# Performance work log

Measured on AMD Instinct MI355X. Metric: run time of the kernel, lower is better.

## Reference

```python
import jax, jax.numpy as jnp
import numpy as np


def setup_inputs() -> dict:
    key = jax.random.key(0)
    k1, k2, k3, k4, k5 = jax.random.split(key, 5)
    N, M = 8192, 8192
    ref_kpts = jax.random.normal(k1, (N, 3), dtype=jnp.float32)
    src_kpts = jax.random.normal(k2, (M, 3), dtype=jnp.float32)
    gt_transform = jax.random.normal(k3, (4, 4), dtype=jnp.float32)
    ref_sigma = jax.random.uniform(k4, (N,), dtype=jnp.float32)
    src_sigma = jax.random.uniform(k5, (M,), dtype=jnp.float32)
    return {"ref_kpts": ref_kpts, "src_kpts": src_kpts, "gt_transform": gt_transform,
            "ref_sigma": ref_sigma, "src_sigma": src_sigma}


def reference(ref_kpts, src_kpts, gt_transform, ref_sigma, src_sigma):
    # apply_transform: rigid SE(3): p @ R^T + t
    R = gt_transform[:3, :3]
    t = gt_transform[:3, 3]
    kpts2 = src_kpts @ R.T + t  # [M, 3]
    # pairwise euclidean distances [N, M]
    diff = jnp.linalg.norm(ref_kpts[:, None, :] - kpts2[None, :, :], axis=-1)
    # forward direction: for each ref point, nearest transformed src point
    min_dist_fwd = jnp.min(diff, axis=-1)        # [N]
    idx_fwd = jnp.argmin(diff, axis=-1)          # [N]
    sigma_fwd = (ref_sigma + src_sigma[idx_fwd]) * 0.5
    forward_loss = jnp.mean(jnp.log(sigma_fwd) + min_dist_fwd / sigma_fwd)
    # backward direction: for each src point, nearest ref point
    min_dist_bwd = jnp.min(diff, axis=0)         # [M]
    idx_bwd = jnp.argmin(diff, axis=0)           # [M]
    sigma_bwd = (src_sigma + ref_sigma[idx_bwd]) * 0.5
    backward_loss = jnp.mean(jnp.log(sigma_bwd) + min_dist_bwd / sigma_bwd)
    return forward_loss + backward_loss
```

## Files before the change

### kernel.cpp

```cpp
#include <hip/hip_runtime.h>
#include <math.h>

typedef float v4f __attribute__((ext_vector_type(4)));

#define TPB 256
#define IPT 8
#define JS  128


__global__ __launch_bounds__(256) void setup_kernel(
    const float* __restrict__ ref, const float* __restrict__ src,
    const float* __restrict__ T,
    float* __restrict__ refI, float* __restrict__ srcI,
    unsigned long long* __restrict__ packF,
    unsigned long long* __restrict__ packB,
    float* __restrict__ out, int N, int M) {
  int i = blockIdx.x * blockDim.x + threadIdx.x;
  if (i < M) {
    float x = src[3 * i], y = src[3 * i + 1], z = src[3 * i + 2];
    float tx = T[0] * x + T[1] * y + T[2]  * z + T[3];
    float ty = T[4] * x + T[5] * y + T[6]  * z + T[7];
    float tz = T[8] * x + T[9] * y + T[10] * z + T[11];
    int base = 8 * (i >> 1) + (i & 1);
    srcI[base]     = tx;
    srcI[base + 2] = ty;
    srcI[base + 4] = tz;
    srcI[base + 6] = tx * tx + ty * ty + tz * tz;
    packB[i] = ~0ull;
  }
  if (i < N) {
    float x = ref[3 * i], y = ref[3 * i + 1], z = ref[3 * i + 2];
    int base = 8 * (i >> 1) + (i & 1);
    refI[base]     = x;
    refI[base + 2] = y;
    refI[base + 4] = z;
    refI[base + 6] = x * x + y * y + z * z;
    packF[i] = ~0ull;
  }
  if (i == 0) {
    out[0] = 0.0f;
#pragma unroll
    for (int e = 0; e < 2; e++) {
      int bn = 8 * ((N + e) >> 1) + ((N + e) & 1);
      refI[bn] = 0.f; refI[bn + 2] = 0.f; refI[bn + 4] = 0.f;
      refI[bn + 6] = 1e30f;
      int bm = 8 * ((M + e) >> 1) + ((M + e) & 1);
      srcI[bm] = 0.f; srcI[bm + 2] = 0.f; srcI[bm + 4] = 0.f;
      srcI[bm + 6] = 1e30f;
    }
  }
}

__device__ __forceinline__ unsigned int sortable(float f) {
  unsigned int u = __float_as_uint(f);
  return u ^ ((unsigned int)((int)u >> 31) | 0x80000000u);
}

__global__ __launch_bounds__(TPB, 4) void pairs_kernel(
    const float* __restrict__ refI, const float* __restrict__ srcI,
    unsigned long long* __restrict__ packF,
    unsigned long long* __restrict__ packB,
    int N, int M, int nbF) {
  int b = blockIdx.x;
  const float *selfI, *otherI;
  unsigned long long* pack;
  int selfN, otherN;
  if (b < nbF) {
    selfI = refI; otherI = srcI; pack = packF; selfN = N; otherN = M;
  } else {
    b -= nbF;
    selfI = srcI; otherI = refI; pack = packB; selfN = M; otherN = N;
  }
  const int ib = b / JS, jb = b % JS;
  const int i0 = ib * (TPB * IPT) + threadIdx.x;

  float ax[IPT], ay[IPT], az[IPT], m0[IPT], m1[IPT];
#pragma unroll
  for (int k = 0; k < IPT; k++) {
    int i = i0 + k * TPB;
    int ic = (i < selfN) ? i : (selfN - 1);
    int base = 8 * (ic >> 1) + (ic & 1);
    ax[k] = -2.0f * selfI[base];
    ay[k] = -2.0f * selfI[base + 2];
    az[k] = -2.0f * selfI[base + 4];
    m0[k] = 1e30f; m1[k] = 1e30f;
  }

  int chunk = (otherN + JS - 1) / JS;
  chunk = (chunk + 1) & ~1;
  const int j0 = jb * chunk;
  const int jcount = min(chunk, otherN - j0);

  const int lowbits = 32 - __clz((chunk > 2 ? chunk : 2) - 1);
  const unsigned keep = ~((1u << lowbits) - 1u);

  const v4f* og = (const v4f*)(otherI + 4 * j0);

#pragma unroll 2
  for (int jj = 0; jj < jcount; jj += 2) {
    v4f A = og[jj];
    v4f B = og[jj + 1];
#pragma unroll
    for (int k = 0; k < IPT; k++) {
      float u0 = __builtin_fmaf(ax[k], A.x, B.z);
      u0 = __builtin_fmaf(ay[k], A.z, u0);
      u0 = __builtin_fmaf(az[k], B.x, u0);
      float u1 = __builtin_fmaf(ax[k], A.y, B.w);
      u1 = __builtin_fmaf(ay[k], A.w, u1);
      u1 = __builtin_fmaf(az[k], B.y, u1);
      float e0 = __uint_as_float((__float_as_uint(u0) & keep) | (unsigned)jj);
      float e1 = __uint_as_float((__float_as_uint(u1) & keep) |
                                 (unsigned)(jj + 1));
      m0[k] = fminf(m0[k], e0);
      m1[k] = fminf(m1[k], e1);
    }
  }

#pragma unroll
  for (int k = 0; k < IPT; k++) {
    int i = i0 + k * TPB;
    if (i < selfN && jcount > 0) {
      float mf = fminf(m0[k], m1[k]);
      unsigned mb = __float_as_uint(mf);
      int jloc = (int)(mb & ~keep);
      unsigned long long p = ((unsigned long long)sortable(mf) << 32) |
                             (unsigned int)(j0 + jloc);
      atomicMin(&pack[i], p);
    }
  }
}

__global__ __launch_bounds__(256) void finalize_kernel(
    const unsigned long long* __restrict__ packF,
    const unsigned long long* __restrict__ packB,
    const float* __restrict__ refI, const float* __restrict__ srcI,
    const float* __restrict__ ref_sigma, const float* __restrict__ src_sigma,
    float* __restrict__ out, int N, int M) {
  int gid = blockIdx.x * blockDim.x + threadIdx.x;
  float term = 0.f;
  if (gid < N) {
    int idx = (int)(packF[gid] & 0xffffffffu);
    int sb = 8 * (gid >> 1) + (gid & 1);
    int ob = 8 * (idx >> 1) + (idx & 1);
    float dx = refI[sb]     - srcI[ob];
    float dy = refI[sb + 2] - srcI[ob + 2];
    float dz = refI[sb + 4] - srcI[ob + 4];
    float d = sqrtf(dx * dx + dy * dy + dz * dz);
    float sigma = 0.5f * (ref_sigma[gid] + src_sigma[idx]);
    term = (logf(sigma) + d / sigma) * (1.0f / (float)N);
  } else if (gid < N + M) {
    int j = gid - N;
    int idx = (int)(packB[j] & 0xffffffffu);
    int sb = 8 * (j >> 1) + (j & 1);
    int ob = 8 * (idx >> 1) + (idx & 1);
    float dx = srcI[sb]     - refI[ob];
    float dy = srcI[sb + 2] - refI[ob + 2];
    float dz = srcI[sb + 4] - refI[ob + 4];
    float d = sqrtf(dx * dx + dy * dy + dz * dz);
    float sigma = 0.5f * (src_sigma[j] + ref_sigma[idx]);
    term = (logf(sigma) + d / sigma) * (1.0f / (float)M);
  }
#pragma unroll
  for (int o = 32; o > 0; o >>= 1) term += __shfl_down(term, o, 64);
  __shared__ float wsum[4];
  const int lane = threadIdx.x & 63, wid = threadIdx.x >> 6;
  if (lane == 0) wsum[wid] = term;
  __syncthreads();
  if (threadIdx.x == 0)
    atomicAdd(out, wsum[0] + wsum[1] + wsum[2] + wsum[3]);
}

extern "C" void kernel_launch(void* const* d_in, const int* in_sizes, int n_in,
                              void* d_out, int out_size, void* d_ws,
                              size_t ws_size, hipStream_t stream) {
  const float* ref_kpts  = (const float*)d_in[0];
  const float* src_kpts  = (const float*)d_in[1];
  const float* gt        = (const float*)d_in[2];
  const float* ref_sigma = (const float*)d_in[3];
  const float* src_sigma = (const float*)d_in[4];
  float* out = (float*)d_out;

  const int N = in_sizes[0] / 3;
  const int M = in_sizes[1] / 3;

  const int NG8 = 8 * ((N + 3) / 2);
  const int MG8 = 8 * ((M + 3) / 2);
  float* f = (float*)d_ws;
  float* refI = f;
  float* srcI = f + NG8;
  unsigned long long* packF = (unsigned long long*)(f + NG8 + MG8);
  unsigned long long* packB = packF + N;

  int nPts = (N > M) ? N : M;
  setup_kernel<<<(nPts + 255) / 256, 256, 0, stream>>>(
      ref_kpts, src_kpts, gt, refI, srcI, packF, packB, out, N, M);

  const int ibF = (N + TPB * IPT - 1) / (TPB * IPT);
  const int ibB = (M + TPB * IPT - 1) / (TPB * IPT);
  const int nbF = ibF * JS;
  const int nbB = ibB * JS;
  pairs_kernel<<<nbF + nbB, TPB, 0, stream>>>(refI, srcI, packF, packB,
                                              N, M, nbF);

  finalize_kernel<<<(N + M + 255) / 256, 256, 0, stream>>>(
      packF, packB, refI, srcI, ref_sigma, src_sigma, out, N, M);
}
```

Baseline: 90.27 us.

## Fuse point transform into pairs kernel, stage tiles in LDS, replace atomics with partials

Drops the separate setup kernel. The pairs kernel now reads the raw ref/src points, applies the rigid transform on the fly, and stages each chunk of other-points with their squared norms into a shared-memory tile. Instead of 64-bit atomicMin into one packed array, each block writes its per-point min key to a partial buffer indexed by j-block. The finalize kernel reduces the 128 partials per point before computing the loss. This removes a launch and the atomic contention. In exchange it adds roughly 16 MB of partial-buffer traffic, redundant transform math in every block, and __syncthreads around the tile loads.

After: 92.66 us. 1.03x slower.

```diff
diff --git a/kernel.cpp b/kernel.cpp
--- a/kernel.cpp
+++ b/kernel.cpp
@@ -6,71 +6,52 @@
 #define TPB 256
 #define IPT 8
 #define JS  128
-
-
-__global__ __launch_bounds__(256) void setup_kernel(
-    const float* __restrict__ ref, const float* __restrict__ src,
-    const float* __restrict__ T,
-    float* __restrict__ refI, float* __restrict__ srcI,
-    unsigned long long* __restrict__ packF,
-    unsigned long long* __restrict__ packB,
-    float* __restrict__ out, int N, int M) {
-  int i = blockIdx.x * blockDim.x + threadIdx.x;
-  if (i < M) {
-    float x = src[3 * i], y = src[3 * i + 1], z = src[3 * i + 2];
-    float tx = T[0] * x + T[1] * y + T[2]  * z + T[3];
-    float ty = T[4] * x + T[5] * y + T[6]  * z + T[7];
-    float tz = T[8] * x + T[9] * y + T[10] * z + T[11];
-    int base = 8 * (i >> 1) + (i & 1);
-    srcI[base]     = tx;
-    srcI[base + 2] = ty;
-    srcI[base + 4] = tz;
-    srcI[base + 6] = tx * tx + ty * ty + tz * tz;
-    packB[i] = ~0ull;
-  }
-  if (i < N) {
-    float x = ref[3 * i], y = ref[3 * i + 1], z = ref[3 * i + 2];
-    int base = 8 * (i >> 1) + (i & 1);
-    refI[base]     = x;
-    refI[base + 2] = y;
-    refI[base + 4] = z;
-    refI[base + 6] = x * x + y * y + z * z;
-    packF[i] = ~0ull;
-  }
-  if (i == 0) {
-    out[0] = 0.0f;
-#pragma unroll
-    for (int e = 0; e < 2; e++) {
-      int bn = 8 * ((N + e) >> 1) + ((N + e) & 1);
-      refI[bn] = 0.f; refI[bn + 2] = 0.f; refI[bn + 4] = 0.f;
-      refI[bn + 6] = 1e30f;
-      int bm = 8 * ((M + e) >> 1) + ((M + e) & 1);
-      srcI[bm] = 0.f; srcI[bm + 2] = 0.f; srcI[bm + 4] = 0.f;
-      srcI[bm + 6] = 1e30f;
-    }
-  }
-}
+#define TS  512
+
 
 __device__ __forceinline__ unsigned int sortable(float f) {
   unsigned int u = __float_as_uint(f);
   return u ^ ((unsigned int)((int)u >> 31) | 0x80000000u);
 }
 
+struct Xform {
+  float t0, t1, t2, t3, t4, t5, t6, t7, t8, t9, t10, t11;
+};
+
+__device__ __forceinline__ Xform load_xform(const float* __restrict__ T) {
+  Xform X = {T[0], T[1], T[2], T[3], T[4],  T[5],
+             T[6], T[7], T[8], T[9], T[10], T[11]};
+  return X;
+}
+
+__device__ __forceinline__ void apply_xform(const Xform& X, float& x, float& y,
+                                            float& z) {
+  float tx = X.t0 * x + X.t1 * y + X.t2 * z + X.t3;
+  float ty = X.t4 * x + X.t5 * y + X.t6 * z + X.t7;
+  float tz = X.t8 * x + X.t9 * y + X.t10 * z + X.t11;
+  x = tx; y = ty; z = tz;
+}
+
 __global__ __launch_bounds__(TPB, 4) void pairs_kernel(
-    const float* __restrict__ refI, const float* __restrict__ srcI,
-    unsigned long long* __restrict__ packF,
-    unsigned long long* __restrict__ packB,
-    int N, int M, int nbF) {
-  int b = blockIdx.x;
-  const float *selfI, *otherI;
-  unsigned long long* pack;
-  int selfN, otherN;
-  if (b < nbF) {
-    selfI = refI; otherI = srcI; pack = packF; selfN = N; otherN = M;
-  } else {
-    b -= nbF;
-    selfI = srcI; otherI = refI; pack = packB; selfN = M; otherN = N;
-  }
+    const float* __restrict__ ref, const float* __restrict__ src,
+    const float* __restrict__ T,
+    unsigned long long* __restrict__ partF,
+    unsigned long long* __restrict__ partB,
+    float* __restrict__ out, int N, int M, int nbF) {
+  __shared__ __align__(16) float tile[TS * 4];
+  const int b0 = blockIdx.x;
+  if (b0 == 0 && threadIdx.x == 0) out[0] = 0.0f;
+
+  const Xform X = load_xform(T);
+
+  const bool fwd = (b0 < nbF);
+  const int b = fwd ? b0 : b0 - nbF;
+  const float* selfP  = fwd ? ref : src;
+  const float* otherP = fwd ? src : ref;
+  unsigned long long* part = fwd ? partF : partB;
+  const int selfN  = fwd ? N : M;
+  const int otherN = fwd ? M : N;
+
   const int ib = b / JS, jb = b % JS;
   const int i0 = ib * (TPB * IPT) + threadIdx.x;
 
@@ -79,10 +60,9 @@
   for (int k = 0; k < IPT; k++) {
     int i = i0 + k * TPB;
     int ic = (i < selfN) ? i : (selfN - 1);
-    int base = 8 * (ic >> 1) + (ic & 1);
-    ax[k] = -2.0f * selfI[base];
-    ay[k] = -2.0f * selfI[base + 2];
-    az[k] = -2.0f * selfI[base + 4];
+    float x = selfP[3 * ic], y = selfP[3 * ic + 1], z = selfP[3 * ic + 2];
+    if (!fwd) apply_xform(X, x, y, z);
+    ax[k] = -2.0f * x; ay[k] = -2.0f * y; az[k] = -2.0f * z;
     m0[k] = 1e30f; m1[k] = 1e30f;
   }
 
@@ -94,68 +74,107 @@
   const int lowbits = 32 - __clz((chunk > 2 ? chunk : 2) - 1);
   const unsigned keep = ~((1u << lowbits) - 1u);
 
-  const v4f* og = (const v4f*)(otherI + 4 * j0);
-
-#pragma unroll 2
-  for (int jj = 0; jj < jcount; jj += 2) {
-    v4f A = og[jj];
-    v4f B = og[jj + 1];
-#pragma unroll
-    for (int k = 0; k < IPT; k++) {
-      float u0 = __builtin_fmaf(ax[k], A.x, B.z);
-      u0 = __builtin_fmaf(ay[k], A.z, u0);
-      u0 = __builtin_fmaf(az[k], B.x, u0);
-      float u1 = __builtin_fmaf(ax[k], A.y, B.w);
-      u1 = __builtin_fmaf(ay[k], A.w, u1);
-      u1 = __builtin_fmaf(az[k], B.y, u1);
-      float e0 = __uint_as_float((__float_as_uint(u0) & keep) | (unsigned)jj);
-      float e1 = __uint_as_float((__float_as_uint(u1) & keep) |
-                                 (unsigned)(jj + 1));
-      m0[k] = fminf(m0[k], e0);
-      m1[k] = fminf(m1[k], e1);
-    }
+  for (int jt = 0; jt < jcount; jt += TS) {
+    const int tc = min(TS, jcount - jt);
+    const int tce = (tc + 1) & ~1;
+    for (int t = threadIdx.x; t < tce; t += TPB) {
+      int j = j0 + jt + t;
+      float x = 0.f, y = 0.f, z = 0.f, w = 1e30f;
+      if (j < otherN) {
+        x = otherP[3 * j]; y = otherP[3 * j + 1]; z = otherP[3 * j + 2];
+        if (fwd) apply_xform(X, x, y, z);
+        w = x * x + y * y + z * z;
+      }
+      tile[4 * t] = x; tile[4 * t + 1] = y;
+      tile[4 * t + 2] = z; tile[4 * t + 3] = w;
+    }
+    __syncthreads();
+#pragma unroll 4
+    for (int jj = 0; jj < tce; jj += 2) {
+      v4f A = *(const v4f*)&tile[4 * jj];
+      v4f B = *(const v4f*)&tile[4 * jj + 4];
+      const unsigned ej0 = (unsigned)(jt + jj);
+      const unsigned ej1 = (unsigned)(jt + jj + 1);
+#pragma unroll
+      for (int k = 0; k < IPT; k++) {
+        float u0 = __builtin_fmaf(ax[k], A.x, A.w);
+        u0 = __builtin_fmaf(ay[k], A.y, u0);
+        u0 = __builtin_fmaf(az[k], A.z, u0);
+        float u1 = __builtin_fmaf(ax[k], B.x, B.w);
+        u1 = __builtin_fmaf(ay[k], B.y, u1);
+        u1 = __builtin_fmaf(az[k], B.z, u1);
+        float e0 = __uint_as_float((__float_as_uint(u0) & keep) | ej0);
+        float e1 = __uint_as_float((__float_as_uint(u1) & keep) | ej1);
+        m0[k] = fminf(m0[k], e0);
+        m1[k] = fminf(m1[k], e1);
+      }
+    }
+    __syncthreads();
   }
 
 #pragma unroll
   for (int k = 0; k < IPT; k++) {
     int i = i0 + k * TPB;
-    if (i < selfN && jcount > 0) {
-      float mf = fminf(m0[k], m1[k]);
-      unsigned mb = __float_as_uint(mf);
-      int jloc = (int)(mb & ~keep);
-      unsigned long long p = ((unsigned long long)sortable(mf) << 32) |
-                             (unsigned int)(j0 + jloc);
-      atomicMin(&pack[i], p);
+    if (i < selfN) {
+      unsigned long long key;
+      if (jcount > 0) {
+        float mf = fminf(m0[k], m1[k]);
+        unsigned mb = __float_as_uint(mf);
+        unsigned jloc = mb & ~keep;
+        key = ((unsigned long long)sortable(mf) << 32) |
+              (unsigned)(j0 + (int)jloc);
+      } else {
+        key = ~0ull;
+      }
+      part[(size_t)jb * selfN + i] = key;
     }
   }
 }
 
 __global__ __launch_bounds__(256) void finalize_kernel(
-    const unsigned long long* __restrict__ packF,
-    const unsigned long long* __restrict__ packB,
-    const float* __restrict__ refI, const float* __restrict__ srcI,
+    const unsigned long long* __restrict__ partF,
+    const unsigned long long* __restrict__ partB,
+    const float* __restrict__ ref, const float* __restrict__ src,
+    const float* __restrict__ T,
     const float* __restrict__ ref_sigma, const float* __restrict__ src_sigma,
     float* __restrict__ out, int N, int M) {
   int gid = blockIdx.x * blockDim.x + threadIdx.x;
+  const Xform X = load_xform(T);
   float term = 0.f;
   if (gid < N) {
-    int idx = (int)(packF[gid] & 0xffffffffu);
-    int sb = 8 * (gid >> 1) + (gid & 1);
-    int ob = 8 * (idx >> 1) + (idx & 1);
-    float dx = refI[sb]     - srcI[ob];
-    float dy = refI[sb + 2] - srcI[ob + 2];
-    float dz = refI[sb + 4] - srcI[ob + 4];
+    unsigned long long ma = ~0ull, mb = ~0ull;
+#pragma unroll 8
+    for (int s = 0; s < JS; s += 2) {
+      unsigned long long k0 = partF[(size_t)s * N + gid];
+      unsigned long long k1 = partF[(size_t)(s + 1) * N + gid];
+      ma = (k0 < ma) ? k0 : ma;
+      mb = (k1 < mb) ? k1 : mb;
+    }
+    unsigned long long m = (ma < mb) ? ma : mb;
+    int idx = (int)(m & 0xffffffffu);
+    float x = src[3 * idx], y = src[3 * idx + 1], z = src[3 * idx + 2];
+    apply_xform(X, x, y, z);
+    float dx = ref[3 * gid] - x, dy = ref[3 * gid + 1] - y,
+          dz = ref[3 * gid + 2] - z;
     float d = sqrtf(dx * dx + dy * dy + dz * dz);
     float sigma = 0.5f * (ref_sigma[gid] + src_sigma[idx]);
     term = (logf(sigma) + d / sigma) * (1.0f / (float)N);
   } else if (gid < N + M) {
     int j = gid - N;
-    int idx = (int)(packB[j] & 0xffffffffu);
-    int sb = 8 * (j >> 1) + (j & 1);
-    int ob = 8 * (idx >> 1) + (idx & 1);
-    float dx = srcI[sb]     - refI[ob];
-    float dy = srcI[sb + 2] - refI[ob + 2];
-    float dz = srcI[sb + 4] - refI[ob + 4];
+    unsigned long long ma = ~0ull, mb = ~0ull;
+#pragma unroll 8
+    for (int s = 0; s < JS; s += 2) {
+      unsigned long long k0 = partB[(size_t)s * M + j];
+      unsigned long long k1 = partB[(size_t)(s + 1) * M + j];
+      ma = (k0 < ma) ? k0 : ma;
+      mb = (k1 < mb) ? k1 : mb;
+    }
+    unsigned long long m = (ma < mb) ? ma : mb;
+    int idx = (int)(m & 0xffffffffu);
+    float x = src[3 * j], y = src[3 * j + 1], z = src[3 * j + 2];
+    apply_xform(X, x, y, z);
+    float dx = x - ref[3 * idx], dy = y - ref[3 * idx + 1],
+          dz = z - ref[3 * idx + 2];
     float d = sqrtf(dx * dx + dy * dy + dz * dz);
     float sigma = 0.5f * (src_sigma[j] + ref_sigma[idx]);
     term = (logf(sigma) + d / sigma) * (1.0f / (float)M);
@@ -183,25 +202,16 @@
   const int N = in_sizes[0] / 3;
   const int M = in_sizes[1] / 3;
 
-  const int NG8 = 8 * ((N + 3) / 2);
-  const int MG8 = 8 * ((M + 3) / 2);
-  float* f = (float*)d_ws;
-  float* refI = f;
-  float* srcI = f + NG8;
-  unsigned long long* packF = (unsigned long long*)(f + NG8 + MG8);
-  unsigned long long* packB = packF + N;
-
-  int nPts = (N > M) ? N : M;
-  setup_kernel<<<(nPts + 255) / 256, 256, 0, stream>>>(
-      ref_kpts, src_kpts, gt, refI, srcI, packF, packB, out, N, M);
+  unsigned long long* partF = (unsigned long long*)d_ws;
+  unsigned long long* partB = partF + (size_t)JS * N;
 
   const int ibF = (N + TPB * IPT - 1) / (TPB * IPT);
   const int ibB = (M + TPB * IPT - 1) / (TPB * IPT);
   const int nbF = ibF * JS;
   const int nbB = ibB * JS;
-  pairs_kernel<<<nbF + nbB, TPB, 0, stream>>>(refI, srcI, packF, packB,
-                                              N, M, nbF);
+  pairs_kernel<<<nbF + nbB, TPB, 0, stream>>>(ref_kpts, src_kpts, gt, partF,
+                                              partB, out, N, M, nbF);
 
   finalize_kernel<<<(N + M + 255) / 256, 256, 0, stream>>>(
-      packF, packB, refI, srcI, ref_sigma, src_sigma, out, N, M);
-}
+      partF, partB, ref_kpts, src_kpts, gt, ref_sigma, src_sigma, out, N, M);
+}
```
